# Performance work log

Measured on AMD Instinct MI355X. Metric: run time of the kernel, lower is better.

Reference implementation:

```python
import jax, jax.numpy as jnp
import numpy as np
from jax import lax

K = 16
EPS = 1e-5


def setup_inputs() -> dict:
    key = jax.random.key(0)
    k1, k2, k3 = jax.random.split(key, 3)
    x = jax.random.normal(k1, (8, 4096, 64), jnp.float32)
    pos = jax.random.normal(k2, (8, 4096, 3), jnp.float32)
    # nn.Linear(64,128), xavier_uniform weight, zero bias
    limit = float(np.sqrt(6.0 / (64 + 128)))
    W = jax.random.uniform(k3, (128, 64), jnp.float32, -limit, limit)
    b = jnp.zeros((128,), jnp.float32)
    gamma = jnp.ones((128,), jnp.float32)   # BN weight
    beta = jnp.zeros((128,), jnp.float32)   # BN bias
    return {"x": x, "pos": pos, "W": W, "b": b, "gamma": gamma, "beta": beta,
            "n_sampling": 1024}


def _fps(pos3, n_sampling):
    """Farthest point sampling starting at index 0. pos3: [bz,N,3] -> [bz,S] int32."""
    bz, N, _ = pos3.shape

    def step(carry, _):
        min_d, last = carry                                   # [bz,N], [bz]
        lastp = jnp.take_along_axis(pos3, last[:, None, None], axis=1)  # [bz,1,3]
        d = jnp.sum((pos3 - lastp) ** 2, axis=-1)             # [bz,N]
        min_d = jnp.minimum(min_d, d)
        nxt = jnp.argmax(min_d, axis=1).astype(jnp.int32)
        return (min_d, nxt), last

    init = (jnp.full((bz, N), 1e10, pos3.dtype), jnp.zeros((bz,), jnp.int32))
    _, idx = lax.scan(step, init, None, length=n_sampling)    # [S,bz]
    return idx.T                                              # [bz,S]


def _knn_idx(pos3, fps_idx, k):
    """k nearest neighbors (by squared L2) of sampled points among all N points."""
    spos = jnp.take_along_axis(pos3, fps_idx[..., None], axis=1)        # [bz,S,3]
    # ||a-b||^2 = |a|^2 + |b|^2 - 2 a.b, avoids [bz,S,N,3] intermediate
    d = (jnp.sum(spos ** 2, -1)[:, :, None]
         + jnp.sum(pos3 ** 2, -1)[:, None, :]
         - 2.0 * jnp.einsum('bsd,bnd->bsn', spos, pos3))               # [bz,S,N]
    _, idx = lax.top_k(-d, k)                                           # [bz,S,k]
    return idx


def reference(x, pos, W, b, gamma, beta, n_sampling):
    pos3 = pos[..., :3]
    fps_idx = _fps(pos3, n_sampling)                          # [bz,S]
    knn_idx = _knn_idx(pos3, fps_idx, K)                      # [bz,S,K]

    # Linear -> BatchNorm1d (training-mode batch stats, biased var) -> ReLU
    h = jnp.einsum('bnf,of->bno', x, W) + b                   # [bz,N,128]
    mean = h.mean(axis=(0, 1))
    var = h.var(axis=(0, 1))
    h = (h - mean) / jnp.sqrt(var + EPS) * gamma + beta
    h = jax.nn.relu(h)

    # gather k-NN features and max-pool (same math as expand+repeat+gather+max)
    gathered = jax.vmap(lambda hb, ib: hb[ib])(h, knn_idx)    # [bz,S,K,128]
    sampled_knn_x = gathered.max(axis=2)                      # [bz,S,128]

    sampled_pos = jnp.take_along_axis(pos, fps_idx[..., None], axis=1)  # [bz,S,3]
    return sampled_knn_x, sampled_pos
```

## Files before the change

### kernel.cpp

```cpp
#include <hip/hip_runtime.h>
#include <stdint.h>

typedef unsigned long long ull;
typedef float f32x2 __attribute__((ext_vector_type(2)));

#define NBATCH 8
#define NPTS   4096
#define NS     1024
#define NK     16
#define NF     64
#define NO     128

#define FT  256
#define PPT 16

static __device__ __forceinline__ ull umax64(ull a, ull b) { return a > b ? a : b; }

__global__ __launch_bounds__(256) void fps_stats_kernel(
    const float* __restrict__ pos, const float* __restrict__ x,
    const float* __restrict__ W, const float* __restrict__ bias,
    int* __restrict__ fps_idx, float* __restrict__ out_pos,
    float* __restrict__ partial) {
#pragma clang fp contract(off)
  const int t = threadIdx.x;
  __shared__ float plds[NPTS * 3];
  __shared__ __align__(16) ull wslot[2][4];
  __shared__ int widx_lds[NS];

  if (blockIdx.x >= 8) {
    const int blk = blockIdx.x - 8;
    const int c = t & 127;
    const int h = t >> 7;
    float* xl = plds;

    const float4* Wv = (const float4*)(W + c * NF);
    float4 w[16];
#pragma unroll
    for (int q = 0; q < 16; ++q) w[q] = Wv[q];
    const float bb = bias[c];

    const float4* src = (const float4*)(x + (size_t)blk * 128 * NF);
    float4* dst = (float4*)xl;
    for (int i = t; i < 128 * NF / 4; i += 256) dst[i] = src[i];
    __syncthreads();

    float s = 0.f, s2 = 0.f;
    for (int r = h * 64; r < h * 64 + 64; ++r) {
      const float4* xr = (const float4*)(xl + r * NF);
      float hh = bb;
#pragma unroll
      for (int q = 0; q < 16; ++q) {
        const float4 xv = xr[q];
        hh = fmaf(xv.x, w[q].x, hh);
        hh = fmaf(xv.y, w[q].y, hh);
        hh = fmaf(xv.z, w[q].z, hh);
        hh = fmaf(xv.w, w[q].w, hh);
      }
      s += hh;
      s2 = fmaf(hh, hh, s2);
    }
    partial[(blk * 2 + h) * 256 + c] = s;
    partial[(blk * 2 + h) * 256 + 128 + c] = s2;
    return;
  }

  const int b = blockIdx.x;
  const float* p = pos + (size_t)b * NPTS * 3;
  {
    const float4* src = (const float4*)p;
    float4* dst = (float4*)plds;
    for (int i = t; i < NPTS * 3 / 4; i += FT) dst[i] = src[i];
  }
  if (t == 0) widx_lds[0] = 0;
  __syncthreads();

  f32x2 px2[PPT / 2], py2[PPT / 2], pz2[PPT / 2], md2[PPT / 2];
#pragma unroll
  for (int jp = 0; jp < PPT / 2; ++jp) {
    const int i0 = t + FT * (2 * jp);
    const int i1 = i0 + FT;
    px2[jp] = (f32x2){plds[3 * i0 + 0], plds[3 * i1 + 0]};
    py2[jp] = (f32x2){plds[3 * i0 + 1], plds[3 * i1 + 1]};
    pz2[jp] = (f32x2){plds[3 * i0 + 2], plds[3 * i1 + 2]};
    md2[jp] = (f32x2){1e10f, 1e10f};
  }

  float lx = plds[0], ly = plds[1], lz = plds[2];

  for (int s = 1; s < NS; ++s) {
    const f32x2 lxv = (f32x2){lx, lx};
    const f32x2 lyv = (f32x2){ly, ly};
    const f32x2 lzv = (f32x2){lz, lz};
    f32x2 acc = (f32x2){0.f, 0.f};
#pragma unroll
    for (int jp = 0; jp < PPT / 2; ++jp) {
      const f32x2 dx = px2[jp] - lxv;
      const f32x2 dy = py2[jp] - lyv;
      const f32x2 dz = pz2[jp] - lzv;
      const f32x2 xx = dx * dx;
      const f32x2 yy = dy * dy;
      const f32x2 zz = dz * dz;
      const f32x2 sxy = xx + yy;
      const f32x2 d = sxy + zz;
      md2[jp] = __builtin_elementwise_min(md2[jp], d);
      acc = __builtin_elementwise_max(acc, md2[jp]);
    }
    float best = fmaxf(acc.x, acc.y);
    int lidx = 0;
#pragma unroll
    for (int jp = 0; jp < PPT / 2; ++jp) {
      if (md2[jp].x == best) lidx = t + FT * (2 * jp);
      if (md2[jp].y == best) lidx = t + FT * (2 * jp) + FT;
    }
#define CARRY_STEP(ctrl)                                                     \
    {                                                                        \
      const float bo = __int_as_float(__builtin_amdgcn_update_dpp(           \
          0, __float_as_int(best), ctrl, 0xf, 0xf, true));                   \
      const int io =                                                         \
          __builtin_amdgcn_update_dpp(0, lidx, ctrl, 0xf, 0xf, true);        \
      if (bo > best) {        \
        best = bo;                                                           \
        lidx = io;                                                           \
      }                                                                      \
    }
    CARRY_STEP(0x111)
    CARRY_STEP(0x112)
    CARRY_STEP(0x114)
    CARRY_STEP(0x118)
    CARRY_STEP(0x142)
    CARRY_STEP(0x143)
#undef CARRY_STEP
    if ((t & 63) == 63)
      wslot[s & 1][t >> 6] = ((ull)__float_as_uint(best) << 32) | (unsigned)lidx;
    __syncthreads();
    const ull* wk = wslot[s & 1];
    const ull kk =
        umax64(umax64(wk[0], wk[1]), umax64(wk[2], wk[3]));
    const int widx = (int)(kk & 0xFFFFFFFFu);
    lx = plds[3 * widx + 0];
    ly = plds[3 * widx + 1];
    lz = plds[3 * widx + 2];
    if (t == 0) widx_lds[s] = widx;
  }

  __syncthreads();
  for (int i = t; i < NS; i += FT) {
    const int wi = widx_lds[i];
    fps_idx[b * NS + i] = wi;
    out_pos[((size_t)b * NS + i) * 3 + 0] = plds[3 * wi + 0];
    out_pos[((size_t)b * NS + i) * 3 + 1] = plds[3 * wi + 1];
    out_pos[((size_t)b * NS + i) * 3 + 2] = plds[3 * wi + 2];
  }
}

__global__ __launch_bounds__(1024) void stats_reduce_kernel(
    const float* __restrict__ partial, const float* __restrict__ gamma,
    const float* __restrict__ beta, float* __restrict__ ab) {
  const int t = threadIdx.x;
  const int c = t & 127;
  const int q = t >> 7;
  __shared__ double sred[1024], s2red[1024];
  double s = 0.0, s2 = 0.0;
#pragma unroll 4
  for (int r = q * 64; r < q * 64 + 64; ++r) {
    s += (double)partial[r * 256 + c];
    s2 += (double)partial[r * 256 + 128 + c];
  }
  sred[t] = s;
  s2red[t] = s2;
  __syncthreads();
  if (t < 128) {
    s = 0.0;
    s2 = 0.0;
#pragma unroll
    for (int qq = 0; qq < 8; ++qq) {
      s += sred[qq * 128 + t];
      s2 += s2red[qq * 128 + t];
    }
    const double n = 32768.0;
    const double mean = s / n;
    const double var = s2 / n - mean * mean;
    const float inv = (float)(1.0 / sqrt(var + 1e-5));
    const float scale = gamma[t] * inv;
    const float shift = beta[t] - (float)mean * scale;
    ab[t] = scale;
    ab[128 + t] = shift;
  }
}

__global__ __launch_bounds__(256) void knn_gather_kernel(
    const float* __restrict__ pos, const int* __restrict__ fps_idx,
    const float* __restrict__ x, const float* __restrict__ W,
    const float* __restrict__ bias, const float* __restrict__ ab,
    float* __restrict__ out) {
  __shared__ ull sbuf[NPTS * 3 / 2];
  __shared__ int il2[32 * NK];
  float* plds = (float*)sbuf;
  const int b = blockIdx.y;
  const int t = threadIdx.x;

  const float* p = pos + (size_t)b * NPTS * 3;
  for (int i = t; i < NPTS * 3; i += 256) plds[i] = p[i];
  __syncthreads();

  {
    const int samp = blockIdx.x * 32 + (t >> 3);
    const int chunk = t & 7;
    const int sidx = fps_idx[b * NS + samp];
    const float sx = plds[sidx * 3 + 0];
    const float sy = plds[sidx * 3 + 1];
    const float sz = plds[sidx * 3 + 2];

    ull keys[16];
#pragma unroll
    for (int k = 0; k < 16; ++k) keys[k] = 0xFFFFFFFF00000000ull | (unsigned)k;
    ull worst = 0xFFFFFFFF0000000Full;

    for (int j = 0; j < 512; ++j) {
      const int i = j * 8 + chunk;
      const float dx = plds[i * 3 + 0] - sx;
      const float dy = plds[i * 3 + 1] - sy;
      const float dz = plds[i * 3 + 2] - sz;
      const float d = dx * dx + dy * dy + dz * dz;
      const ull key = ((ull)__float_as_uint(d) << 32) | (unsigned)i;
      if (key < worst) {
#pragma unroll
        for (int k = 0; k < 16; ++k) keys[k] = (keys[k] == worst) ? key : keys[k];
        ull w = keys[0];
#pragma unroll
        for (int k = 1; k < 16; ++k) w = umax64(w, keys[k]);
        worst = w;
      }
    }
    __syncthreads();
#pragma unroll
    for (int k = 0; k < 16; ++k) sbuf[t * 16 + k] = keys[k];
    __syncthreads();

    if (t < 32) {
      ull best[16];
#pragma unroll
      for (int k = 0; k < 16; ++k)
        best[k] = 0xFFFFFFFF00000000ull | (unsigned)(64 + k);
      ull w = 0xFFFFFFFF00000000ull | (unsigned)(64 + 15);
      for (int c = 0; c < 8; ++c) {
#pragma unroll
        for (int k = 0; k < 16; ++k) {
          const ull key = sbuf[(t * 8 + c) * 16 + k];
          if (key < w) {
#pragma unroll
            for (int q = 0; q < 16; ++q) best[q] = (best[q] == w) ? key : best[q];
            ull nw = best[0];
#pragma unroll
            for (int q = 1; q < 16; ++q) nw = umax64(nw, best[q]);
            w = nw;
          }
        }
      }
#pragma unroll
      for (int k = 0; k < 16; ++k)
        il2[t * NK + k] = (int)(best[k] & 0xFFFFFFFFu);
    }
  }

  const int c2 = t & 63;
  const int g = t >> 6;
  float4 w0[16], w1[16];
  {
    const float4* Wv0 = (const float4*)(W + c2 * NF);
    const float4* Wv1 = (const float4*)(W + (c2 + 64) * NF);
#pragma unroll
    for (int q = 0; q < 16; ++q) {
      w0[q] = Wv0[q];
      w1[q] = Wv1[q];
    }
  }
  const float bb0 = bias[c2], bb1 = bias[c2 + 64];
  const float scale0 = ab[c2], scale1 = ab[c2 + 64];
  const float shift0 = ab[128 + c2], shift1 = ab[128 + c2 + 64];

  float* xl = (float*)sbuf;
  const float* xb = x + (size_t)b * NPTS * NF;

  for (int pass = 0; pass < 4; ++pass) {
    __syncthreads();
    {
      const int r = t & 127;
      const int q0 = (t >> 7) * 8;
      const int idx = il2[(pass * 8 + (r >> 4)) * NK + (r & 15)];
      const float4* srow = (const float4*)(xb + (size_t)idx * NF) + q0;
      float4* drow = (float4*)(xl + r * NF) + q0;
#pragma unroll
      for (int q = 0; q < 8; ++q) drow[q] = srow[q];
    }
    __syncthreads();

#pragma unroll
    for (int sg = 0; sg < 2; ++sg) {
      const int ss = 2 * g + sg;
      float m0 = 0.0f, m1 = 0.0f;
#pragma unroll
      for (int k = 0; k < NK; ++k) {
        const float4* xr = (const float4*)(xl + (ss * 16 + k) * NF);
        float h0 = bb0, h1 = bb1;
#pragma unroll
        for (int q = 0; q < 16; ++q) {
          const float4 xv = xr[q];
          h0 = fmaf(xv.x, w0[q].x, h0);
          h0 = fmaf(xv.y, w0[q].y, h0);
          h0 = fmaf(xv.z, w0[q].z, h0);
          h0 = fmaf(xv.w, w0[q].w, h0);
          h1 = fmaf(xv.x, w1[q].x, h1);
          h1 = fmaf(xv.y, w1[q].y, h1);
          h1 = fmaf(xv.z, w1[q].z, h1);
          h1 = fmaf(xv.w, w1[q].w, h1);
        }
        h0 = fmaf(h0, scale0, shift0);
        h1 = fmaf(h1, scale1, shift1);
        h0 = h0 > 0.f ? h0 : 0.f;
        h1 = h1 > 0.f ? h1 : 0.f;
        m0 = m0 > h0 ? m0 : h0;
        m1 = m1 > h1 ? m1 : h1;
      }
      float* o = out + ((size_t)b * NS + blockIdx.x * 32 + pass * 8 + ss) * NO;
      o[c2] = m0;
      o[c2 + 64] = m1;
    }
  }
}

extern "C" void kernel_launch(void* const* d_in, const int* in_sizes, int n_in,
                              void* d_out, int out_size, void* d_ws, size_t ws_size,
                              hipStream_t stream) {
  const float* x     = (const float*)d_in[0];
  const float* pos   = (const float*)d_in[1];
  const float* W     = (const float*)d_in[2];
  const float* bias  = (const float*)d_in[3];
  const float* gamma = (const float*)d_in[4];
  const float* beta  = (const float*)d_in[5];

  float* out_knn = (float*)d_out;
  float* out_pos = out_knn + (size_t)NBATCH * NS * NO;

  char* ws = (char*)d_ws;
  int* fps_idx   = (int*)(ws);
  float* partial = (float*)(ws + (32 << 10));
  float* ab      = (float*)(ws + (544 << 10));

  fps_stats_kernel<<<8 + 256, 256, 0, stream>>>(pos, x, W, bias, fps_idx,
                                                out_pos, partial);
  stats_reduce_kernel<<<1, 1024, 0, stream>>>(partial, gamma, beta, ab);
  knn_gather_kernel<<<dim3(32, NBATCH), 256, 0, stream>>>(pos, fps_idx, x, W,
                                                          bias, ab, out_knn);
}
```

Measured before the change: 1.090 ms.

## Split kNN across 16 threads per sample and double the block grid

The kNN gather kernel now processes 16 samples per block instead of 32, giving 512 blocks instead of 256. Each sample's 4096-point scan is split over 16 threads instead of 8, and one thread per sample merges the 256 partial candidates. The kernel also uses float4 loads for positions, fused-FMA distances and a tree-shaped max for the worst key. This is meant to fill the GPU better and shorten per-thread scan loops, at the cost of a longer serial merge and W being reloaded by twice as many blocks. The FPS stage, which likely dominates, is unchanged.

```diff
diff --git a/kernel.cpp b/kernel.cpp
--- a/kernel.cpp
+++ b/kernel.cpp
@@ -15,6 +15,14 @@
 #define PPT 16
 
 static __device__ __forceinline__ ull umax64(ull a, ull b) { return a > b ? a : b; }
+
+static __device__ __forceinline__ float dist2(const float* plds, int i, float sx,
+                                              float sy, float sz) {
+  const float dx = plds[i * 3 + 0] - sx;
+  const float dy = plds[i * 3 + 1] - sy;
+  const float dz = plds[i * 3 + 2] - sz;
+  return fmaf(dz, dz, fmaf(dy, dy, dx * dx));
+}
 
 __global__ __launch_bounds__(256) void fps_stats_kernel(
     const float* __restrict__ pos, const float* __restrict__ x,
@@ -118,7 +126,7 @@
           0, __float_as_int(best), ctrl, 0xf, 0xf, true));                   \
       const int io =                                                         \
           __builtin_amdgcn_update_dpp(0, lidx, ctrl, 0xf, 0xf, true);        \
-      if (bo > best) {        \
+      if (bo > best) {                                                       \
         best = bo;                                                           \
         lidx = io;                                                           \
       }                                                                      \
@@ -134,8 +142,7 @@
       wslot[s & 1][t >> 6] = ((ull)__float_as_uint(best) << 32) | (unsigned)lidx;
     __syncthreads();
     const ull* wk = wslot[s & 1];
-    const ull kk =
-        umax64(umax64(wk[0], wk[1]), umax64(wk[2], wk[3]));
+    const ull kk = umax64(umax64(wk[0], wk[1]), umax64(wk[2], wk[3]));
     const int widx = (int)(kk & 0xFFFFFFFFu);
     lx = plds[3 * widx + 0];
     ly = plds[3 * widx + 1];
@@ -193,74 +200,73 @@
     const float* __restrict__ x, const float* __restrict__ W,
     const float* __restrict__ bias, const float* __restrict__ ab,
     float* __restrict__ out) {
-  __shared__ ull sbuf[NPTS * 3 / 2];
-  __shared__ int il2[32 * NK];
-  float* plds = (float*)sbuf;
+  __shared__ ull smem[10240];
+  float* plds = (float*)smem;
+  ull* keys = smem + 6144;
   const int b = blockIdx.y;
   const int t = threadIdx.x;
-
-  const float* p = pos + (size_t)b * NPTS * 3;
-  for (int i = t; i < NPTS * 3; i += 256) plds[i] = p[i];
-  __syncthreads();
+  const int s0 = blockIdx.x * 16;
 
   {
-    const int samp = blockIdx.x * 32 + (t >> 3);
-    const int chunk = t & 7;
-    const int sidx = fps_idx[b * NS + samp];
-    const float sx = plds[sidx * 3 + 0];
-    const float sy = plds[sidx * 3 + 1];
-    const float sz = plds[sidx * 3 + 2];
-
-    ull keys[16];
-#pragma unroll
-    for (int k = 0; k < 16; ++k) keys[k] = 0xFFFFFFFF00000000ull | (unsigned)k;
+    const float4* src = (const float4*)(pos + (size_t)b * NPTS * 3);
+    float4* dst = (float4*)plds;
+    for (int i = t; i < NPTS * 3 / 4; i += 256) dst[i] = src[i];
+  }
+  __syncthreads();
+
+  const int samp = t >> 4;
+  const int chunk = t & 15;
+  const int sidx = fps_idx[b * NS + s0 + samp];
+  const float sx = plds[sidx * 3 + 0];
+  const float sy = plds[sidx * 3 + 1];
+  const float sz = plds[sidx * 3 + 2];
+
+  {
+    ull k16[16];
+#pragma unroll
+    for (int k = 0; k < 16; ++k) k16[k] = 0xFFFFFFFF00000000ull | (unsigned)k;
     ull worst = 0xFFFFFFFF0000000Full;
-
-    for (int j = 0; j < 512; ++j) {
-      const int i = j * 8 + chunk;
-      const float dx = plds[i * 3 + 0] - sx;
-      const float dy = plds[i * 3 + 1] - sy;
-      const float dz = plds[i * 3 + 2] - sz;
-      const float d = dx * dx + dy * dy + dz * dz;
+    for (int j = 0; j < 256; ++j) {
+      const int i = j * 16 + chunk;
+      const float d = dist2(plds, i, sx, sy, sz);
       const ull key = ((ull)__float_as_uint(d) << 32) | (unsigned)i;
       if (key < worst) {
 #pragma unroll
-        for (int k = 0; k < 16; ++k) keys[k] = (keys[k] == worst) ? key : keys[k];
-        ull w = keys[0];
-#pragma unroll
-        for (int k = 1; k < 16; ++k) w = umax64(w, keys[k]);
-        worst = w;
+        for (int k = 0; k < 16; ++k) k16[k] = (k16[k] == worst) ? key : k16[k];
+        ull w01 = umax64(k16[0], k16[1]);
+        ull w2 = umax64(umax64(k16[2], k16[3]), umax64(k16[4], k16[5]));
+        ull w3 = umax64(umax64(k16[6], k16[7]), umax64(k16[8], k16[9]));
+        ull w4 = umax64(umax64(k16[10], k16[11]), umax64(k16[12], k16[13]));
+        ull w5 = umax64(k16[14], k16[15]);
+        worst = umax64(umax64(w01, w2), umax64(w3, umax64(w4, w5)));
       }
     }
-    __syncthreads();
-#pragma unroll
-    for (int k = 0; k < 16; ++k) sbuf[t * 16 + k] = keys[k];
-    __syncthreads();
-
-    if (t < 32) {
-      ull best[16];
-#pragma unroll
-      for (int k = 0; k < 16; ++k)
-        best[k] = 0xFFFFFFFF00000000ull | (unsigned)(64 + k);
-      ull w = 0xFFFFFFFF00000000ull | (unsigned)(64 + 15);
-      for (int c = 0; c < 8; ++c) {
-#pragma unroll
-        for (int k = 0; k < 16; ++k) {
-          const ull key = sbuf[(t * 8 + c) * 16 + k];
-          if (key < w) {
-#pragma unroll
-            for (int q = 0; q < 16; ++q) best[q] = (best[q] == w) ? key : best[q];
-            ull nw = best[0];
-#pragma unroll
-            for (int q = 1; q < 16; ++q) nw = umax64(nw, best[q]);
-            w = nw;
-          }
-        }
+#pragma unroll
+    for (int k = 0; k < 16; ++k) keys[(chunk * 16 + k) * 16 + samp] = k16[k];
+  }
+  __syncthreads();
+
+  if (t < 16) {
+    ull best[16];
+#pragma unroll
+    for (int k = 0; k < 16; ++k)
+      best[k] = 0xFFFFFFFF00000000ull | (unsigned)(4096 + k);
+    ull w = 0xFFFFFFFF00000000ull | (unsigned)(4096 + 15);
+    for (int j = 0; j < 256; ++j) {
+      const ull key = keys[j * 16 + t];
+      if (key < w) {
+#pragma unroll
+        for (int q = 0; q < 16; ++q) best[q] = (best[q] == w) ? key : best[q];
+        ull a0 = umax64(best[0], best[1]);
+        ull a1 = umax64(umax64(best[2], best[3]), umax64(best[4], best[5]));
+        ull a2 = umax64(umax64(best[6], best[7]), umax64(best[8], best[9]));
+        ull a3 = umax64(umax64(best[10], best[11]), umax64(best[12], best[13]));
+        ull a4 = umax64(best[14], best[15]);
+        w = umax64(umax64(a0, a1), umax64(a2, umax64(a3, a4)));
       }
-#pragma unroll
-      for (int k = 0; k < 16; ++k)
-        il2[t * NK + k] = (int)(best[k] & 0xFFFFFFFFu);
-    }
+    }
+#pragma unroll
+    for (int k = 0; k < 16; ++k) keys[k * 16 + t] = best[k];
   }
 
   const int c2 = t & 63;
@@ -279,53 +285,50 @@
   const float scale0 = ab[c2], scale1 = ab[c2 + 64];
   const float shift0 = ab[128 + c2], shift1 = ab[128 + c2 + 64];
 
-  float* xl = (float*)sbuf;
+  float* xtile = (float*)smem;
   const float* xb = x + (size_t)b * NPTS * NF;
 
   for (int pass = 0; pass < 4; ++pass) {
     __syncthreads();
     {
-      const int r = t & 127;
-      const int q0 = (t >> 7) * 8;
-      const int idx = il2[(pass * 8 + (r >> 4)) * NK + (r & 15)];
-      const float4* srow = (const float4*)(xb + (size_t)idx * NF) + q0;
-      float4* drow = (float4*)(xl + r * NF) + q0;
-#pragma unroll
-      for (int q = 0; q < 8; ++q) drow[q] = srow[q];
+      const int r = t & 63;
+      const int q0 = (t >> 6) * 4;
+      const int idx =
+          (int)(keys[(r & 15) * 16 + (pass * 4 + (r >> 4))] & 0xFFFFFFFFu);
+      const float4* srow = (const float4*)(xb + (size_t)idx * NF);
+      float4* drow = (float4*)(xtile + r * NF);
+#pragma unroll
+      for (int q = q0; q < q0 + 4; ++q) drow[q] = srow[q];
     }
     __syncthreads();
 
-#pragma unroll
-    for (int sg = 0; sg < 2; ++sg) {
-      const int ss = 2 * g + sg;
-      float m0 = 0.0f, m1 = 0.0f;
-#pragma unroll
-      for (int k = 0; k < NK; ++k) {
-        const float4* xr = (const float4*)(xl + (ss * 16 + k) * NF);
-        float h0 = bb0, h1 = bb1;
-#pragma unroll
-        for (int q = 0; q < 16; ++q) {
-          const float4 xv = xr[q];
-          h0 = fmaf(xv.x, w0[q].x, h0);
-          h0 = fmaf(xv.y, w0[q].y, h0);
-          h0 = fmaf(xv.z, w0[q].z, h0);
-          h0 = fmaf(xv.w, w0[q].w, h0);
-          h1 = fmaf(xv.x, w1[q].x, h1);
-          h1 = fmaf(xv.y, w1[q].y, h1);
-          h1 = fmaf(xv.z, w1[q].z, h1);
-          h1 = fmaf(xv.w, w1[q].w, h1);
-        }
-        h0 = fmaf(h0, scale0, shift0);
-        h1 = fmaf(h1, scale1, shift1);
-        h0 = h0 > 0.f ? h0 : 0.f;
-        h1 = h1 > 0.f ? h1 : 0.f;
-        m0 = m0 > h0 ? m0 : h0;
-        m1 = m1 > h1 ? m1 : h1;
+    float m0 = 0.0f, m1 = 0.0f;
+#pragma unroll
+    for (int k = 0; k < NK; ++k) {
+      const float4* xr = (const float4*)(xtile + (g * 16 + k) * NF);
+      float h0 = bb0, h1 = bb1;
+#pragma unroll
+      for (int q = 0; q < 16; ++q) {
+        const float4 xv = xr[q];
+        h0 = fmaf(xv.x, w0[q].x, h0);
+        h0 = fmaf(xv.y, w0[q].y, h0);
+        h0 = fmaf(xv.z, w0[q].z, h0);
+        h0 = fmaf(xv.w, w0[q].w, h0);
+        h1 = fmaf(xv.x, w1[q].x, h1);
+        h1 = fmaf(xv.y, w1[q].y, h1);
+        h1 = fmaf(xv.z, w1[q].z, h1);
+        h1 = fmaf(xv.w, w1[q].w, h1);
       }
-      float* o = out + ((size_t)b * NS + blockIdx.x * 32 + pass * 8 + ss) * NO;
-      o[c2] = m0;
-      o[c2 + 64] = m1;
-    }
+      h0 = fmaf(h0, scale0, shift0);
+      h1 = fmaf(h1, scale1, shift1);
+      h0 = h0 > 0.f ? h0 : 0.f;
+      h1 = h1 > 0.f ? h1 : 0.f;
+      m0 = m0 > h0 ? m0 : h0;
+      m1 = m1 > h1 ? m1 : h1;
+    }
+    float* o = out + ((size_t)b * NS + s0 + pass * 4 + g) * NO;
+    o[c2] = m0;
+    o[c2 + 64] = m1;
   }
 }
 
@@ -350,6 +353,6 @@
   fps_stats_kernel<<<8 + 256, 256, 0, stream>>>(pos, x, W, bias, fps_idx,
                                                 out_pos, partial);
   stats_reduce_kernel<<<1, 1024, 0, stream>>>(partial, gamma, beta, ab);
-  knn_gather_kernel<<<dim3(32, NBATCH), 256, 0, stream>>>(pos, fps_idx, x, W,
+  knn_gather_kernel<<<dim3(64, NBATCH), 256, 0, stream>>>(pos, fps_idx, x, W,
                                                           bias, ab, out_knn);
 }
```

Measured after the change: 1.178 ms. +8.1%, slower.
